# Performance work log

Measured on AMD Instinct MI355X. Metric: run time of the kernel, lower is better.

## Reference

```python
import jax, jax.numpy as jnp
import numpy as np

N_ANCHORS = 10647
N_CLASSES = 80
N_OUT = 5 + N_CLASSES
N_GT = 2048
POS_IOU = 0.7
NEG_IOU = 0.3
N_SAMPLE = 256
POS_RATIO = 0.5


def _cxcy_to_corners(b):
    return jnp.concatenate([b[:, :2] - b[:, 2:4] / 2, b[:, :2] + b[:, 2:4] / 2], axis=-1)


def _iou(a, b):
    # a: [N,4] corner boxes, b: [M,4] corner boxes -> [N,M]
    lt = jnp.maximum(a[:, None, :2], b[None, :, :2])
    rb = jnp.minimum(a[:, None, 2:], b[None, :, 2:])
    wh = jnp.clip(rb - lt, 0.0)
    inter = wh[..., 0] * wh[..., 1]
    area_a = (a[:, 2] - a[:, 0]) * (a[:, 3] - a[:, 1])
    area_b = (b[:, 2] - b[:, 0]) * (b[:, 3] - b[:, 1])
    return inter / (area_a[:, None] + area_b[None, :] - inter)


def _bce_logits(x, t):
    # numerically stable BCEWithLogits, elementwise
    return jnp.maximum(x, 0.0) - x * t + jnp.log1p(jnp.exp(-jnp.abs(x)))


def _demote_first(labels, value, excess):
    # demote the first `excess` anchors (in index order) whose label == value to -1,
    # mirroring torch's nonzero()[randperm(excess)] which always hits the first
    # `excess` entries of the nonzero list
    m = labels == value
    cum = jnp.cumsum(m.astype(jnp.int32))
    return jnp.where(m & (cum <= excess), -1.0, labels)


def _generate_targets(priors, gt_boxes, gt_labels):
    ious = _iou(_cxcy_to_corners(priors[:, :4]), _cxcy_to_corners(gt_boxes))  # [N, M]
    gt_max_index = jnp.argmax(ious, axis=0)       # [M] best anchor per gt
    anchor_max_ious = jnp.max(ious, axis=1)       # [N]
    anchor_max_index = jnp.argmax(ious, axis=1)   # [N]
    labels = jnp.full((N_ANCHORS,), -1.0, dtype=ious.dtype)
    labels = labels.at[gt_max_index].set(1.0)
    labels = jnp.where(anchor_max_ious >= POS_IOU, 1.0, labels)
    labels = jnp.where(anchor_max_ious < NEG_IOU, 0.0, labels)
    n_pos_quota = int(POS_RATIO * N_SAMPLE)
    n_pos_actual = jnp.sum(labels == 1.0)
    labels = _demote_first(labels, 1.0, jnp.maximum(n_pos_actual - n_pos_quota, 0))
    n_neg_req = N_SAMPLE - jnp.sum(labels == 1.0)
    n_neg_actual = jnp.sum(labels == 0.0)
    labels = _demote_first(labels, 0.0, jnp.maximum(n_neg_actual - n_neg_req, 0))
    anchor_gt_box = gt_boxes[anchor_max_index]    # [N,4] matched gt box per anchor
    anchor_cls = gt_labels[anchor_max_index] + 5  # [N] one-hot class column per anchor
    targets = jnp.zeros((N_ANCHORS, N_OUT), dtype=gt_boxes.dtype)
    targets = targets.at[:, :4].set(anchor_gt_box)
    targets = targets.at[:, 4].set(labels)
    targets = targets.at[jnp.arange(N_ANCHORS), anchor_cls].set(1.0)
    return targets


def _forward(predictions, gt_boxes, gt_labels, priors):
    targets = _generate_targets(priors, gt_boxes, gt_labels)
    pred = predictions[0]                          # [N, N_OUT]
    labels = targets[:, 4]
    pos = (labels == 1.0).astype(pred.dtype)
    neg = (labels == 0.0).astype(pred.dtype)
    n_pos = jnp.maximum(jnp.sum(pos), 1.0)
    n_neg = jnp.maximum(jnp.sum(neg), 1.0)
    # masked-mean MSE over x,y,w,h on positive anchors
    diff2 = (pred[:, :4] - targets[:, :4]) ** 2
    loss_box = jnp.sum(pos[:, None] * diff2, axis=0) / n_pos
    loss_conf_obj = jnp.sum(pos * _bce_logits(pred[:, 4], targets[:, 4])) / n_pos
    loss_conf_nonobj = jnp.sum(neg * _bce_logits(pred[:, 4], targets[:, 4])) / n_neg
    loss_class = jnp.sum(pos[:, None] * _bce_logits(pred[:, 5:], targets[:, 5:])) / (n_pos * N_CLASSES)
    total_loss = jnp.sum(loss_box) + loss_conf_obj + loss_conf_nonobj + loss_class
    return pred, total_loss


def setup_inputs() -> dict:
    key = jax.random.key(0)
    k1, k2, k3, k4 = jax.random.split(key, 4)
    predictions = jax.random.normal(k1, (1, N_ANCHORS, N_OUT), dtype=jnp.float32)
    gt_boxes = jax.random.uniform(k2, (N_GT, 4), dtype=jnp.float32, minval=0.05, maxval=0.95)
    gt_labels = jax.random.randint(k3, (N_GT,), 0, N_CLASSES)
    priors = jax.random.uniform(k4, (N_ANCHORS, N_OUT), dtype=jnp.float32, minval=0.05, maxval=0.95)
    return {"predictions": predictions, "gt_boxes": gt_boxes, "gt_labels": gt_labels, "priors": priors}


def reference(predictions, gt_boxes, gt_labels, priors):
    return _forward(predictions, gt_boxes, gt_labels, priors)
```

## Files before the change

### kernel.cpp

```cpp
#include <hip/hip_runtime.h>
#include <math.h>

#define N_ANCH 10647
#define N_GT   2048
#define N_OUTC 85
#define PRED_ELEMS (N_ANCH * N_OUTC)
#define PRED_V4    (PRED_ELEMS / 4)
#define N_CHUNK    42

#define ABX 21
#define ABY 32
#define NBLK_A (ABX * ABY)
#define GBX 4
#define GBY 167
#define NBLK_G (GBX * GBY)
#define NBLK_IOU (NBLK_A + NBLK_G)
#define CPY_PER_BLK ((PRED_V4 + NBLK_IOU - 1) / NBLK_IOU)

struct WS {
    unsigned long long akey[N_ANCH];
    unsigned long long gkey[N_GT];
    int cnt_p[N_CHUNK], cnt_n[N_CHUNK];
    unsigned int sync;
};

__device__ __forceinline__ float bce(float x, float t) {
    return fmaxf(x, 0.0f) - x * t + log1pf(expf(-fabsf(x)));
}

__device__ __forceinline__ unsigned long long packkey(float iou, int idx) {
    return ((unsigned long long)__float_as_uint(iou) << 32) |
           (unsigned)(~(unsigned)idx);
}

__global__ __launch_bounds__(256) void k_iou(const float* __restrict__ pred,
                                             const float* __restrict__ gtb,
                                             const float* __restrict__ priors,
                                             float* __restrict__ out,
                                             WS* __restrict__ ws) {
    int b = blockIdx.x, t = threadIdx.x;
    if (t < CPY_PER_BLK) {
        int idx = b * CPY_PER_BLK + t;
        if (idx < PRED_V4)
            ((float4*)out)[idx] = ((const float4*)pred)[idx];
    }
    if (b == 0 && t == 0) {
        out[PRED_ELEMS - 3] = pred[PRED_ELEMS - 3];
        out[PRED_ELEMS - 2] = pred[PRED_ELEMS - 2];
        out[PRED_ELEMS - 1] = pred[PRED_ELEMS - 1];
        out[PRED_ELEMS] = 0.0f;
    }

    __shared__ float4 sc[64];
    __shared__ float  sa[64];

    if (b < NBLK_A) {
        int bx = b % ABX, by = b / ABX;
        int jbase = by * 64;
        if (t < 64) {
            float4 v = ((const float4*)gtb)[jbase + t];
            float4 c = make_float4(v.x - v.z*0.5f, v.y - v.w*0.5f,
                                   v.x + v.z*0.5f, v.y + v.w*0.5f);
            sc[t] = c;
            sa[t] = (c.z - c.x) * (c.w - c.y);
        }
        int i0 = bx * 512 + t, i1 = i0 + 256;
        bool v0 = (i0 < N_ANCH), v1 = (i1 < N_ANCH);
        float4 a0 = make_float4(0.f,0.f,0.f,0.f), a1 = a0;
        float aa0 = 0.f, aa1 = 0.f;
        if (v0) {
            float cx = priors[i0*N_OUTC+0], cy = priors[i0*N_OUTC+1];
            float w  = priors[i0*N_OUTC+2], h  = priors[i0*N_OUTC+3];
            a0 = make_float4(cx - w*0.5f, cy - h*0.5f, cx + w*0.5f, cy + h*0.5f);
            aa0 = (a0.z - a0.x) * (a0.w - a0.y);
        }
        if (v1) {
            float cx = priors[i1*N_OUTC+0], cy = priors[i1*N_OUTC+1];
            float w  = priors[i1*N_OUTC+2], h  = priors[i1*N_OUTC+3];
            a1 = make_float4(cx - w*0.5f, cy - h*0.5f, cx + w*0.5f, cy + h*0.5f);
            aa1 = (a1.z - a1.x) * (a1.w - a1.y);
        }
        __syncthreads();
        float I0 = -1.f, S0 = 1.f, I1 = -1.f, S1 = 1.f;
        int bj0 = 0, bj1 = 0;
#pragma unroll 4
        for (int jj = 0; jj < 64; ++jj) {
            float4 g = sc[jj]; float ga = sa[jj];
            float lx = fmaxf(a0.x, g.x), ly = fmaxf(a0.y, g.y);
            float rx = fminf(a0.z, g.z), ry = fminf(a0.w, g.w);
            float In = fmaxf(rx - lx, 0.f) * fmaxf(ry - ly, 0.f);
            float Sn = aa0 + ga;
            bool c = In * S0 > I0 * Sn;
            I0 = c ? In : I0; S0 = c ? Sn : S0; bj0 = c ? jj : bj0;
            lx = fmaxf(a1.x, g.x); ly = fmaxf(a1.y, g.y);
            rx = fminf(a1.z, g.z); ry = fminf(a1.w, g.w);
            In = fmaxf(rx - lx, 0.f) * fmaxf(ry - ly, 0.f);
            Sn = aa1 + ga;
            c = In * S1 > I1 * Sn;
            I1 = c ? In : I1; S1 = c ? Sn : S1; bj1 = c ? jj : bj1;
        }
        if (v0) atomicMax(&ws->akey[i0], packkey(I0 / (S0 - I0), jbase + bj0));
        if (v1) atomicMax(&ws->akey[i1], packkey(I1 / (S1 - I1), jbase + bj1));
    } else {
        int b2 = b - NBLK_A;
        int bx = b2 % GBX, by = b2 / GBX;
        int ibase = by * 64;
        if (t < 64) {
            int i = ibase + t;
            float4 c = make_float4(0.f, 0.f, 0.f, 0.f);
            float ar = 0.f;
            if (i < N_ANCH) {
                float cx = priors[i*N_OUTC+0], cy = priors[i*N_OUTC+1];
                float w  = priors[i*N_OUTC+2], h  = priors[i*N_OUTC+3];
                c = make_float4(cx - w*0.5f, cy - h*0.5f, cx + w*0.5f, cy + h*0.5f);
                ar = (c.z - c.x) * (c.w - c.y);
            }
            sc[t] = c; sa[t] = ar;
        }
        int j0 = bx * 512 + t, j1 = j0 + 256;
        float4 v = ((const float4*)gtb)[j0];
        float4 g0 = make_float4(v.x - v.z*0.5f, v.y - v.w*0.5f,
                                v.x + v.z*0.5f, v.y + v.w*0.5f);
        float ga0 = (g0.z - g0.x) * (g0.w - g0.y);
        v = ((const float4*)gtb)[j1];
        float4 g1 = make_float4(v.x - v.z*0.5f, v.y - v.w*0.5f,
                                v.x + v.z*0.5f, v.y + v.w*0.5f);
        float ga1 = (g1.z - g1.x) * (g1.w - g1.y);
        __syncthreads();
        float I0 = -1.f, S0 = 1.f, I1 = -1.f, S1 = 1.f;
        int bi0 = 0, bi1 = 0;
#pragma unroll 4
        for (int ii = 0; ii < 64; ++ii) {
            float4 a = sc[ii]; float aa = sa[ii];
            float lx = fmaxf(a.x, g0.x), ly = fmaxf(a.y, g0.y);
            float rx = fminf(a.z, g0.z), ry = fminf(a.w, g0.w);
            float In = fmaxf(rx - lx, 0.f) * fmaxf(ry - ly, 0.f);
            float Sn = aa + ga0;
            bool c = In * S0 > I0 * Sn;
            I0 = c ? In : I0; S0 = c ? Sn : S0; bi0 = c ? ii : bi0;
            lx = fmaxf(a.x, g1.x); ly = fmaxf(a.y, g1.y);
            rx = fminf(a.z, g1.z); ry = fminf(a.w, g1.w);
            In = fmaxf(rx - lx, 0.f) * fmaxf(ry - ly, 0.f);
            Sn = aa + ga1;
            c = In * S1 > I1 * Sn;
            I1 = c ? In : I1; S1 = c ? Sn : S1; bi1 = c ? ii : bi1;
        }
        atomicMax(&ws->gkey[j0], packkey(I0 / (S0 - I0), ibase + bi0));
        atomicMax(&ws->gkey[j1], packkey(I1 / (S1 - I1), ibase + bi1));
    }
}

__global__ __launch_bounds__(256) void k_tail2(const float* __restrict__ pred,
                                               const float* __restrict__ gtb,
                                               const int* __restrict__ gtl,
                                               WS* __restrict__ ws,
                                               float* __restrict__ out) {
    __shared__ int sFlg[256];
    __shared__ int wA[4], wB[4];
    __shared__ int wps[4], wns[4];
    __shared__ int sCp[N_CHUNK], sCn[N_CHUNK];
    __shared__ int    sPosI[256];
    __shared__ float4 sPosBox[256];
    __shared__ int    sPosCls[256];
    __shared__ int    sNegI[256];
    __shared__ float  red[12];
    int b = blockIdx.x, t = threadIdx.x, lane = t & 63, wid = t >> 6;
    int base = b * 256;

    sFlg[t] = 0;
    __syncthreads();
    for (int j = t; j < N_GT; j += 256) {
        int ai = (int)(~(unsigned)(ws->gkey[j]));
        int rel = ai - base;
        if ((unsigned)rel < 256u) sFlg[rel] = 1;
    }
    __syncthreads();
    int i = base + t;
    int lab = -2;
    if (i < N_ANCH) {
        float amax = __uint_as_float((unsigned)(ws->akey[i] >> 32));
        lab = (amax < 0.3f) ? 0 : ((amax >= 0.7f || sFlg[t]) ? 1 : -1);
    }
    bool f1 = (lab == 1), f0 = (lab == 0);
    unsigned long long b1 = __ballot(f1), b0v = __ballot(f0);
    if (lane == 0) { wA[wid] = __popcll(b1); wB[wid] = __popcll(b0v); }
    __syncthreads();
    if (t == 0) {
        int cp = wA[0] + wA[1] + wA[2] + wA[3];
        int cn = wB[0] + wB[1] + wB[2] + wB[3];
        __hip_atomic_store(&ws->cnt_p[b], cp, __ATOMIC_RELAXED, __HIP_MEMORY_SCOPE_AGENT);
        __hip_atomic_store(&ws->cnt_n[b], cn, __ATOMIC_RELAXED, __HIP_MEMORY_SCOPE_AGENT);
        __hip_atomic_fetch_add(&ws->sync, 1u, __ATOMIC_RELEASE, __HIP_MEMORY_SCOPE_AGENT);
        while (__hip_atomic_load(&ws->sync, __ATOMIC_ACQUIRE, __HIP_MEMORY_SCOPE_AGENT)
               < (unsigned)N_CHUNK)
            __builtin_amdgcn_s_sleep(2);
    }
    __syncthreads();
    if (t < N_CHUNK) {
        sCp[t] = __hip_atomic_load(&ws->cnt_p[t], __ATOMIC_ACQUIRE, __HIP_MEMORY_SCOPE_AGENT);
        sCn[t] = __hip_atomic_load(&ws->cnt_n[t], __ATOMIC_ACQUIRE, __HIP_MEMORY_SCOPE_AGENT);
    }
    __syncthreads();
    int npa = 0, nna = 0, pb = 0, nb = 0;
#pragma unroll
    for (int c = 0; c < N_CHUNK; ++c) {
        int cp = sCp[c], cn = sCn[c];
        if (c < b) { pb += cp; nb += cn; }
        npa += cp; nna += cn;
    }
    int excess_pos = (npa > 128) ? (npa - 128) : 0;
    int n_pos_f = npa - excess_pos;
    int n_neg_req = 256 - n_pos_f;
    int excess_neg = (nna > n_neg_req) ? (nna - n_neg_req) : 0;
    int n_neg_f = nna - excess_neg;

    unsigned long long pm = (2ull << lane) - 1ull;
    int r1 = __popcll(b1 & pm), r0 = __popcll(b0v & pm);
    if (lane == 0) { wps[wid] = __popcll(b1); wns[wid] = __popcll(b0v); }
    __syncthreads();
    int p1 = 0, p0 = 0, cpB = 0, cnB = 0;
    for (int w = 0; w < 4; ++w) {
        int v1 = wps[w], v0 = wns[w];
        cpB += v1; cnB += v0;
        if (w < wid) { p1 += v1; p0 += v0; }
    }
    int thp = excess_pos - pb; thp = (thp < 0) ? 0 : thp;
    int thn = excess_neg - nb; thn = (thn < 0) ? 0 : thn;
    if (f1) {
        int L = p1 + r1;
        if (L > thp) {
            int slot = L - thp - 1;
            sPosI[slot] = i;
            unsigned am = ~(unsigned)(ws->akey[i]);
            sPosBox[slot] = ((const float4*)gtb)[am];
            sPosCls[slot] = gtl[am] + 5;
        }
    }
    if (f0) {
        int L = p0 + r0;
        if (L > thn) sNegI[L - thn - 1] = i;
    }
    __syncthreads();
    int nP = cpB - thp; nP = (nP < 0) ? 0 : nP;
    int nN = cnB - thn; nN = (nN < 0) ? 0 : nN;

    float acc_a = 0.f, acc_c = 0.f, acc_n = 0.f;
    int nT = nP * N_OUTC;
    for (int u = t; u < nT; u += 256) {
        int pi = u / N_OUTC, col = u - pi * N_OUTC;
        float p = pred[sPosI[pi] * N_OUTC + col];
        if (col < 4) {
            float d = p - ((const float*)&sPosBox[pi])[col];
            acc_a += d * d;
        } else if (col == 4) {
            acc_a += bce(p, 1.0f);
        } else {
            acc_c += bce(p, (col == sPosCls[pi]) ? 1.0f : 0.0f);
        }
    }
    for (int u = t; u < nN; u += 256)
        acc_n += bce(pred[sNegI[u] * N_OUTC + 4], 0.0f);

    for (int o = 32; o; o >>= 1) {
        acc_a += __shfl_down(acc_a, o);
        acc_c += __shfl_down(acc_c, o);
        acc_n += __shfl_down(acc_n, o);
    }
    if (lane == 0) { red[wid] = acc_a; red[4 + wid] = acc_c; red[8 + wid] = acc_n; }
    __syncthreads();
    if (t == 0) {
        float A  = red[0] + red[1] + red[2]  + red[3];
        float C  = red[4] + red[5] + red[6]  + red[7];
        float Nn = red[8] + red[9] + red[10] + red[11];
        float np = fmaxf((float)n_pos_f, 1.0f);
        float nn = fmaxf((float)n_neg_f, 1.0f);
        float contrib = A / np + Nn / nn + C / (np * 80.0f);
        if (contrib != 0.0f) atomicAdd(&out[PRED_ELEMS], contrib);
    }
}

extern "C" void kernel_launch(void* const* d_in, const int* in_sizes, int n_in,
                              void* d_out, int out_size, void* d_ws, size_t ws_size,
                              hipStream_t stream) {
    const float* pred   = (const float*)d_in[0];
    const float* gtb    = (const float*)d_in[1];
    const int*   gtl    = (const int*)d_in[2];
    const float* priors = (const float*)d_in[3];
    float* out = (float*)d_out;
    WS* ws = (WS*)d_ws;

    hipMemsetAsync(d_ws, 0, sizeof(WS), stream);
    k_iou<<<dim3(NBLK_IOU), 256, 0, stream>>>(pred, gtb, priors, out, ws);
    k_tail2<<<dim3(N_CHUNK), 256, 0, stream>>>(pred, gtb, gtl, ws, out);
}
```

Measured before the change: 66.42 us.

## Fuse IoU and tail kernels into one launch with a grid-wide counter barrier

Merges the IoU/argmax kernel and the label/loss tail kernel into a single kernel. The first 42 blocks wait on a spin barrier built from 8 padded counters until every block has finished its IoU work, then run the tail logic. This removes one kernel launch and the gap between the two kernels. It risks deadlock if the waiting blocks occupy slots that unfinished blocks need, though 1340 blocks should fit co-resident on MI355X, and it adds spin-wait polling.

```diff
diff --git a/kernel.cpp b/kernel.cpp
--- a/kernel.cpp
+++ b/kernel.cpp
@@ -14,14 +14,15 @@
 #define GBX 4
 #define GBY 167
 #define NBLK_G (GBX * GBY)
-#define NBLK_IOU (NBLK_A + NBLK_G)
-#define CPY_PER_BLK ((PRED_V4 + NBLK_IOU - 1) / NBLK_IOU)
+#define NBLK (NBLK_A + NBLK_G)
+#define CPY_PER_BLK ((PRED_V4 + NBLK - 1) / NBLK)
 
 struct WS {
     unsigned long long akey[N_ANCH];
     unsigned long long gkey[N_GT];
     int cnt_p[N_CHUNK], cnt_n[N_CHUNK];
-    unsigned int sync;
+    unsigned int sync1[8 * 32];
+    unsigned int sync2;
 };
 
 __device__ __forceinline__ float bce(float x, float t) {
@@ -33,12 +34,25 @@
            (unsigned)(~(unsigned)idx);
 }
 
-__global__ __launch_bounds__(256) void k_iou(const float* __restrict__ pred,
+__global__ __launch_bounds__(256) void k_all(const float* __restrict__ pred,
                                              const float* __restrict__ gtb,
+                                             const int* __restrict__ gtl,
                                              const float* __restrict__ priors,
                                              float* __restrict__ out,
                                              WS* __restrict__ ws) {
-    int b = blockIdx.x, t = threadIdx.x;
+    __shared__ float4 sc[64];
+    __shared__ float  sa[64];
+    __shared__ int sFlg[256];
+    __shared__ int wA[4], wB[4], wps[4], wns[4];
+    __shared__ int sCp[N_CHUNK], sCn[N_CHUNK];
+    __shared__ int    sPosI[256];
+    __shared__ float4 sPosBox[256];
+    __shared__ int    sPosCls[256];
+    __shared__ int    sNegI[256];
+    __shared__ float  red[12];
+
+    int b = blockIdx.x, t = threadIdx.x, lane = t & 63, wid = t >> 6;
+
     if (t < CPY_PER_BLK) {
         int idx = b * CPY_PER_BLK + t;
         if (idx < PRED_V4)
@@ -50,9 +64,6 @@
         out[PRED_ELEMS - 1] = pred[PRED_ELEMS - 1];
         out[PRED_ELEMS] = 0.0f;
     }
-
-    __shared__ float4 sc[64];
-    __shared__ float  sa[64];
 
     if (b < NBLK_A) {
         int bx = b % ABX, by = b / ABX;
@@ -148,25 +159,28 @@
         atomicMax(&ws->gkey[j0], packkey(I0 / (S0 - I0), ibase + bi0));
         atomicMax(&ws->gkey[j1], packkey(I1 / (S1 - I1), ibase + bi1));
     }
-}
-
-__global__ __launch_bounds__(256) void k_tail2(const float* __restrict__ pred,
-                                               const float* __restrict__ gtb,
-                                               const int* __restrict__ gtl,
-                                               WS* __restrict__ ws,
-                                               float* __restrict__ out) {
-    __shared__ int sFlg[256];
-    __shared__ int wA[4], wB[4];
-    __shared__ int wps[4], wns[4];
-    __shared__ int sCp[N_CHUNK], sCn[N_CHUNK];
-    __shared__ int    sPosI[256];
-    __shared__ float4 sPosBox[256];
-    __shared__ int    sPosCls[256];
-    __shared__ int    sNegI[256];
-    __shared__ float  red[12];
-    int b = blockIdx.x, t = threadIdx.x, lane = t & 63, wid = t >> 6;
+
+    __syncthreads();
+    if (t == 0) {
+        __threadfence();
+        __hip_atomic_fetch_add(&ws->sync1[(b & 7) * 32], 1u,
+                               __ATOMIC_RELEASE, __HIP_MEMORY_SCOPE_AGENT);
+    }
+    if (b >= N_CHUNK) return;
+    if (t == 0) {
+        unsigned tot;
+        do {
+            __builtin_amdgcn_s_sleep(2);
+            tot = 0;
+#pragma unroll
+            for (int k = 0; k < 8; ++k)
+                tot += __hip_atomic_load(&ws->sync1[k * 32],
+                                         __ATOMIC_ACQUIRE, __HIP_MEMORY_SCOPE_AGENT);
+        } while (tot < (unsigned)NBLK);
+    }
+    __syncthreads();
+
     int base = b * 256;
-
     sFlg[t] = 0;
     __syncthreads();
     for (int j = t; j < N_GT; j += 256) {
@@ -190,8 +204,8 @@
         int cn = wB[0] + wB[1] + wB[2] + wB[3];
         __hip_atomic_store(&ws->cnt_p[b], cp, __ATOMIC_RELAXED, __HIP_MEMORY_SCOPE_AGENT);
         __hip_atomic_store(&ws->cnt_n[b], cn, __ATOMIC_RELAXED, __HIP_MEMORY_SCOPE_AGENT);
-        __hip_atomic_fetch_add(&ws->sync, 1u, __ATOMIC_RELEASE, __HIP_MEMORY_SCOPE_AGENT);
-        while (__hip_atomic_load(&ws->sync, __ATOMIC_ACQUIRE, __HIP_MEMORY_SCOPE_AGENT)
+        __hip_atomic_fetch_add(&ws->sync2, 1u, __ATOMIC_RELEASE, __HIP_MEMORY_SCOPE_AGENT);
+        while (__hip_atomic_load(&ws->sync2, __ATOMIC_ACQUIRE, __HIP_MEMORY_SCOPE_AGENT)
                < (unsigned)N_CHUNK)
             __builtin_amdgcn_s_sleep(2);
     }
@@ -290,6 +304,5 @@
     WS* ws = (WS*)d_ws;
 
     hipMemsetAsync(d_ws, 0, sizeof(WS), stream);
-    k_iou<<<dim3(NBLK_IOU), 256, 0, stream>>>(pred, gtb, priors, out, ws);
-    k_tail2<<<dim3(N_CHUNK), 256, 0, stream>>>(pred, gtb, gtl, ws, out);
+    k_all<<<dim3(NBLK), 256, 0, stream>>>(pred, gtb, gtl, priors, out, ws);
 }
```

Result: slower. 83.85 us (+26.2%).

## Precompute anchor and GT corner boxes in a prep kernel replacing memset

Applied to the files above, without the earlier changes.

Adds a small prep kernel that converts priors and GT boxes to corner form with areas once, stores them in the workspace, and zeroes the atomic key arrays and the sync word. This replaces the workspace memset. The IoU kernel now reads the precomputed corners straight from global memory instead of recomputing them in every block and staging them through shared memory, which also removes a __syncthreads. The risks are inner loops that now depend on global/L2 loads rather than LDS, and cnt_p/cnt_n are no longer zeroed, which breaks correctness if the tail kernel accumulates into them.

```diff
diff --git a/kernel.cpp b/kernel.cpp
--- a/kernel.cpp
+++ b/kernel.cpp
@@ -2,6 +2,7 @@
 #include <math.h>
 
 #define N_ANCH 10647
+#define NA_PAD 10688
 #define N_GT   2048
 #define N_OUTC 85
 #define PRED_ELEMS (N_ANCH * N_OUTC)
@@ -18,8 +19,12 @@
 #define CPY_PER_BLK ((PRED_V4 + NBLK_IOU - 1) / NBLK_IOU)
 
 struct WS {
+    float4 ac[NA_PAD];
+    float4 gc[N_GT];
     unsigned long long akey[N_ANCH];
     unsigned long long gkey[N_GT];
+    float aa[NA_PAD];
+    float ga[N_GT];
     int cnt_p[N_CHUNK], cnt_n[N_CHUNK];
     unsigned int sync;
 };
@@ -33,9 +38,35 @@
            (unsigned)(~(unsigned)idx);
 }
 
+__global__ __launch_bounds__(256) void k_prep(const float* __restrict__ gtb,
+                                              const float* __restrict__ priors,
+                                              WS* __restrict__ ws) {
+    int i = blockIdx.x * 256 + threadIdx.x;
+    if (i < NA_PAD) {
+        float4 c = make_float4(0.f, 0.f, 0.f, 0.f);
+        float ar = 0.f;
+        if (i < N_ANCH) {
+            float cx = priors[i*N_OUTC+0], cy = priors[i*N_OUTC+1];
+            float w  = priors[i*N_OUTC+2], h  = priors[i*N_OUTC+3];
+            c = make_float4(cx - w*0.5f, cy - h*0.5f, cx + w*0.5f, cy + h*0.5f);
+            ar = (c.z - c.x) * (c.w - c.y);
+            ws->akey[i] = 0ull;
+        }
+        ws->ac[i] = c;
+        ws->aa[i] = ar;
+    }
+    if (i < N_GT) {
+        float4 v = ((const float4*)gtb)[i];
+        float4 c = make_float4(v.x - v.z*0.5f, v.y - v.w*0.5f,
+                               v.x + v.z*0.5f, v.y + v.w*0.5f);
+        ws->gc[i] = c;
+        ws->ga[i] = (c.z - c.x) * (c.w - c.y);
+        ws->gkey[i] = 0ull;
+    }
+    if (i == 0) ws->sync = 0u;
+}
+
 __global__ __launch_bounds__(256) void k_iou(const float* __restrict__ pred,
-                                             const float* __restrict__ gtb,
-                                             const float* __restrict__ priors,
                                              float* __restrict__ out,
                                              WS* __restrict__ ws) {
     int b = blockIdx.x, t = threadIdx.x;
@@ -51,41 +82,20 @@
         out[PRED_ELEMS] = 0.0f;
     }
 
-    __shared__ float4 sc[64];
-    __shared__ float  sa[64];
-
     if (b < NBLK_A) {
         int bx = b % ABX, by = b / ABX;
         int jbase = by * 64;
-        if (t < 64) {
-            float4 v = ((const float4*)gtb)[jbase + t];
-            float4 c = make_float4(v.x - v.z*0.5f, v.y - v.w*0.5f,
-                                   v.x + v.z*0.5f, v.y + v.w*0.5f);
-            sc[t] = c;
-            sa[t] = (c.z - c.x) * (c.w - c.y);
-        }
         int i0 = bx * 512 + t, i1 = i0 + 256;
         bool v0 = (i0 < N_ANCH), v1 = (i1 < N_ANCH);
-        float4 a0 = make_float4(0.f,0.f,0.f,0.f), a1 = a0;
-        float aa0 = 0.f, aa1 = 0.f;
-        if (v0) {
-            float cx = priors[i0*N_OUTC+0], cy = priors[i0*N_OUTC+1];
-            float w  = priors[i0*N_OUTC+2], h  = priors[i0*N_OUTC+3];
-            a0 = make_float4(cx - w*0.5f, cy - h*0.5f, cx + w*0.5f, cy + h*0.5f);
-            aa0 = (a0.z - a0.x) * (a0.w - a0.y);
-        }
-        if (v1) {
-            float cx = priors[i1*N_OUTC+0], cy = priors[i1*N_OUTC+1];
-            float w  = priors[i1*N_OUTC+2], h  = priors[i1*N_OUTC+3];
-            a1 = make_float4(cx - w*0.5f, cy - h*0.5f, cx + w*0.5f, cy + h*0.5f);
-            aa1 = (a1.z - a1.x) * (a1.w - a1.y);
-        }
-        __syncthreads();
+        int ri0 = v0 ? i0 : 0, ri1 = v1 ? i1 : 0;
+        float4 a0 = ws->ac[ri0]; float aa0 = ws->aa[ri0];
+        float4 a1 = ws->ac[ri1]; float aa1 = ws->aa[ri1];
         float I0 = -1.f, S0 = 1.f, I1 = -1.f, S1 = 1.f;
         int bj0 = 0, bj1 = 0;
 #pragma unroll 4
         for (int jj = 0; jj < 64; ++jj) {
-            float4 g = sc[jj]; float ga = sa[jj];
+            float4 g = ws->gc[jbase + jj];
+            float ga = ws->ga[jbase + jj];
             float lx = fmaxf(a0.x, g.x), ly = fmaxf(a0.y, g.y);
             float rx = fminf(a0.z, g.z), ry = fminf(a0.w, g.w);
             float In = fmaxf(rx - lx, 0.f) * fmaxf(ry - ly, 0.f);
@@ -105,33 +115,15 @@
         int b2 = b - NBLK_A;
         int bx = b2 % GBX, by = b2 / GBX;
         int ibase = by * 64;
-        if (t < 64) {
-            int i = ibase + t;
-            float4 c = make_float4(0.f, 0.f, 0.f, 0.f);
-            float ar = 0.f;
-            if (i < N_ANCH) {
-                float cx = priors[i*N_OUTC+0], cy = priors[i*N_OUTC+1];
-                float w  = priors[i*N_OUTC+2], h  = priors[i*N_OUTC+3];
-                c = make_float4(cx - w*0.5f, cy - h*0.5f, cx + w*0.5f, cy + h*0.5f);
-                ar = (c.z - c.x) * (c.w - c.y);
-            }
-            sc[t] = c; sa[t] = ar;
-        }
         int j0 = bx * 512 + t, j1 = j0 + 256;
-        float4 v = ((const float4*)gtb)[j0];
-        float4 g0 = make_float4(v.x - v.z*0.5f, v.y - v.w*0.5f,
-                                v.x + v.z*0.5f, v.y + v.w*0.5f);
-        float ga0 = (g0.z - g0.x) * (g0.w - g0.y);
-        v = ((const float4*)gtb)[j1];
-        float4 g1 = make_float4(v.x - v.z*0.5f, v.y - v.w*0.5f,
-                                v.x + v.z*0.5f, v.y + v.w*0.5f);
-        float ga1 = (g1.z - g1.x) * (g1.w - g1.y);
-        __syncthreads();
+        float4 g0 = ws->gc[j0]; float ga0 = ws->ga[j0];
+        float4 g1 = ws->gc[j1]; float ga1 = ws->ga[j1];
         float I0 = -1.f, S0 = 1.f, I1 = -1.f, S1 = 1.f;
         int bi0 = 0, bi1 = 0;
 #pragma unroll 4
         for (int ii = 0; ii < 64; ++ii) {
-            float4 a = sc[ii]; float aa = sa[ii];
+            float4 a = ws->ac[ibase + ii];
+            float aa = ws->aa[ibase + ii];
             float lx = fmaxf(a.x, g0.x), ly = fmaxf(a.y, g0.y);
             float rx = fminf(a.z, g0.z), ry = fminf(a.w, g0.w);
             float In = fmaxf(rx - lx, 0.f) * fmaxf(ry - ly, 0.f);
@@ -289,7 +281,7 @@
     float* out = (float*)d_out;
     WS* ws = (WS*)d_ws;
 
-    hipMemsetAsync(d_ws, 0, sizeof(WS), stream);
-    k_iou<<<dim3(NBLK_IOU), 256, 0, stream>>>(pred, gtb, priors, out, ws);
+    k_prep<<<dim3(N_CHUNK), 256, 0, stream>>>(gtb, priors, ws);
+    k_iou<<<dim3(NBLK_IOU), 256, 0, stream>>>(pred, out, ws);
     k_tail2<<<dim3(N_CHUNK), 256, 0, stream>>>(pred, gtb, gtl, ws, out);
 }
```

New measurement: 65.98 us. Within noise of the previous version (-0.7%).
